# Optimization experiments

Measured on AMD Instinct MI355X. Metric: run time of the kernel, lower is better.

## Reference

```python
import jax, jax.numpy as jnp
import numpy as np

# SemiConv2d with semifield_type='MaxMin':
#   out[n,oc,i,j] = max_{ic,kh,kw} min(x_pad[n,ic,i+kh,j+kw], kernel[oc,ic,kh,kw])
# stride=1, 'same' padding with -inf (identity of max).

def setup_inputs() -> dict:
    key = jax.random.key(0)
    kx, kk = jax.random.split(key)
    x = jax.random.normal(kx, (8, 32, 96, 96), dtype=jnp.float32)
    kernel = jax.random.normal(kk, (32, 32, 3, 3), dtype=jnp.float32)
    return {"x": x, "kernel": kernel}


def reference(x, kernel):
    N, IC, H, W = x.shape
    OC, IC2, KH, KW = kernel.shape
    assert IC == IC2
    # same padding for k=3, stride=1 (left=top=1, right=bottom=1)
    p = KH - 1
    top = left = p // 2
    bot = right = p - top
    xp = jnp.pad(x, ((0, 0), (0, 0), (top, bot), (left, right)),
                 constant_values=-jnp.inf)
    out = None
    # small fixed loop over kernel taps (KH*KW = 9); vectorized over N, OC, IC, H, W
    for kh in range(KH):
        for kw in range(KW):
            win = xp[:, :, kh:kh + H, kw:kw + W]           # [N, IC, H, W]
            k_tap = kernel[:, :, kh, kw]                   # [OC, IC]
            # min over values, max over input channels -> [N, OC, H, W]
            v = jnp.max(jnp.minimum(win[:, None], k_tap[None, :, :, None, None]), axis=2)
            out = v if out is None else jnp.maximum(out, v)
    return out
```

## Files before the change

kernel.cpp:

```cpp
#include <hip/hip_runtime.h>
#include <math.h>
#include <stdint.h>


#define HH 96
#define WW 96
#define CIN 32
#define OCN 32
#define XQ_ROWS 98
#define XQ_W 48
#define XQ_SLICE (XQ_ROWS * XQ_W)
#define XQ_TOTAL (256 * XQ_SLICE)
#define TB_TOTAL (32 * 288)
#define WS_NEED ((size_t)XQ_TOTAL * 8 + (size_t)TB_TOTAL * 16)
#define NEGH2 0xFC00FC00u

typedef _Float16 h2 __attribute__((ext_vector_type(2)));
typedef uint32_t u2a4 __attribute__((ext_vector_type(2), aligned(4)));

__device__ __forceinline__ uint32_t pkmin_vs(uint32_t x, uint32_t k) {
    uint32_t d;
    asm("v_pk_min_f16 %0, %1, %2" : "=v"(d) : "v"(x), "s"(k));
    return d;
}
__device__ __forceinline__ uint32_t pkmin_vv(uint32_t a, uint32_t b) {
    uint32_t d;
    asm("v_pk_min_f16 %0, %1, %2" : "=v"(d) : "v"(a), "v"(b));
    return d;
}
__device__ __forceinline__ uint32_t pkmax(uint32_t a, uint32_t b) {
    uint32_t d;
    asm("v_pk_max_f16 %0, %1, %2" : "=v"(d) : "v"(a), "v"(b));
    return d;
}
__device__ __forceinline__ uint32_t packh2(float lo, float hi) {
    h2 p = {(_Float16)lo, (_Float16)hi};
    return __builtin_bit_cast(uint32_t, p);
}

__global__ __launch_bounds__(256) void setup_xq(const float* __restrict__ x,
                                                uint2* __restrict__ xq) {
    int idx = blockIdx.x * 256 + threadIdx.x;
    int j  = idx % XQ_W;
    int t  = idx / XQ_W;
    int hp = t % XQ_ROWS;
    int s  = t / XQ_ROWS;
    int h  = hp - 1;
    bool hv = (h >= 0) && (h < HH);
    const float* row = x + ((size_t)s * HH + (hv ? h : 0)) * WW;
    float a = (hv && j > 0)        ? row[2 * j - 1] : -INFINITY;
    float b = hv                   ? row[2 * j]     : -INFINITY;
    float c = hv                   ? row[2 * j + 1] : -INFINITY;
    float d = (hv && j < XQ_W - 1) ? row[2 * j + 2] : -INFINITY;
    uint2 v;
    v.x = packh2(a, b);
    v.y = packh2(c, d);
    xq[idx] = v;
}

__global__ void setup_tap(const float* __restrict__ kk, uint4* __restrict__ tbl) {
    __shared__ float ks[288];
    const int oc = blockIdx.x;
    const int t  = threadIdx.x;
    float k = kk[oc * 288 + t];
    ks[t] = k;
    __syncthreads();
    int rank = 0;
    for (int s = 0; s < 288; ++s) {
        float kv = ks[s];
        rank += (kv > k) || (kv == k && s < t);
    }
    const int ic = t / 9, tap = t % 9, dh = tap / 3, dw = tap % 3;
    uint32_t off = (uint32_t)(ic * XQ_ROWS + dh) * (XQ_W * 8) + (dw == 2 ? 4u : 0u);
    uint32_t sh  = (dw == 1) ? 16u : 0u;
    tbl[oc * 288 + rank] = make_uint4(packh2(k, k), off, sh, 0u);
}

__device__ __forceinline__ uint32_t tapval(const char* xb, int vbyte, uint4 e) {
    u2a4 q = *(const u2a4*)(xb + e.y + (uint32_t)vbyte);
    uint32_t v = __builtin_amdgcn_alignbit(q.y, q.x, e.z);
    return pkmin_vs(v, e.x);
}

__global__ __launch_bounds__(192, 8) void semiconv_ee(const char* __restrict__ xqb,
                                                      const uint4* __restrict__ tbl,
                                                      float* __restrict__ out) {
    const int tid = threadIdx.x;
    const int jj = tid % 48;
    const int hr = tid / 48;
    const int b  = blockIdx.x;
    const int hp = b % 24;
    const int t  = b / 24;
    const int oc = t & 31;
    const int n  = t >> 5;
    const int h  = hp * 4 + hr;

    const char* xb = xqb + (size_t)n * CIN * XQ_SLICE * 8;
    const int vbyte = (h * XQ_W + jj) * 8;
    const uint4* tb = tbl + oc * 288;

    uint32_t acc = NEGH2;
    uint4 e0 = tb[0], e1 = tb[1], e2 = tb[2], e3 = tb[3];

    for (int c = 0; c < 72; ++c) {
        uint4 f0, f1, f2, f3;
        if (c < 71) {
            const uint4* nb = tb + 4 * (c + 1);
            f0 = nb[0]; f1 = nb[1]; f2 = nb[2]; f3 = nb[3];
        }
        uint32_t m0 = tapval(xb, vbyte, e0);
        uint32_t m1 = tapval(xb, vbyte, e1);
        uint32_t m2 = tapval(xb, vbyte, e2);
        uint32_t m3 = tapval(xb, vbyte, e3);
        acc = pkmax(acc, pkmax(pkmax(m0, m1), pkmax(m2, m3)));

        if (c < 71) {
            uint32_t sw = __builtin_amdgcn_alignbit(acc, acc, 16);
            uint32_t mn = pkmin_vv(acc, sw);
            h2 a  = __builtin_bit_cast(h2, mn);
            h2 kn = __builtin_bit_cast(h2, f0.x);
            if (__all((float)a.x >= (float)kn.x)) break;
            e0 = f0; e1 = f1; e2 = f2; e3 = f3;
        }
    }

    h2 a = __builtin_bit_cast(h2, acc);
    float2 v = make_float2((float)a.x, (float)a.y);
    *(float2*)(out + (((size_t)(n * OCN + oc)) * HH + h) * WW + 2 * jj) = v;
}

#define NEGINF (-INFINITY)
__global__ __launch_bounds__(192, 8) void semiconv2d_f32(
    const float* __restrict__ x, const float* __restrict__ kk, float* __restrict__ out)
{
    const int tid = threadIdx.x;
    const int w  = tid % WW;
    const int hr = tid / WW;
    const int b   = blockIdx.x;
    const int ocb = b & 7;
    const int hp  = (b >> 3) % 48;
    const int n   = (b >> 3) / 48;
    const int h   = hp * 2 + hr;
    const int oc0 = ocb * 4;
    float a0[4], a1[4], a2[4];
#pragma unroll
    for (int i = 0; i < 4; ++i) { a0[i] = NEGINF; a1[i] = NEGINF; a2[i] = NEGINF; }
    const bool vm = (h > 0), vp = (h < HH - 1);
    const int hm  = vm ? h - 1 : h;
    const int hpl = vp ? h + 1 : h;
    const int cm  = (w > 0) ? -1 : 0;
    const int cp  = (w < WW - 1) ? 1 : 0;
    const float* rm = x + ((size_t)(n * CIN) * HH + hm)  * WW + w;
    const float* r1 = x + ((size_t)(n * CIN) * HH + h)   * WW + w;
    const float* rp = x + ((size_t)(n * CIN) * HH + hpl) * WW + w;
#pragma unroll 2
    for (int ic = 0; ic < CIN; ++ic) {
        float r00 = vm ? rm[cm] : NEGINF, r01 = vm ? rm[0] : NEGINF, r02 = vm ? rm[cp] : NEGINF;
        float r10 = r1[cm], r11 = r1[0], r12 = r1[cp];
        float r20 = vp ? rp[cm] : NEGINF, r21 = vp ? rp[0] : NEGINF, r22 = vp ? rp[cp] : NEGINF;
#pragma unroll
        for (int oc = 0; oc < 4; ++oc) {
            const float* kq = kk + (size_t)(((oc0 + oc) * CIN + ic)) * 9;
            a0[oc] = fmaxf(fmaxf(a0[oc], fminf(r00, kq[0])), fmaxf(fminf(r10, kq[3]), fminf(r20, kq[6])));
            a1[oc] = fmaxf(fmaxf(a1[oc], fminf(r01, kq[1])), fmaxf(fminf(r11, kq[4]), fminf(r21, kq[7])));
            a2[oc] = fmaxf(fmaxf(a2[oc], fminf(r02, kq[2])), fmaxf(fminf(r12, kq[5]), fminf(r22, kq[8])));
        }
        rm += HH * WW; r1 += HH * WW; rp += HH * WW;
    }
#pragma unroll
    for (int oc = 0; oc < 4; ++oc) {
        float v0 = (w > 0)      ? a0[oc] : NEGINF;
        float v2 = (w < WW - 1) ? a2[oc] : NEGINF;
        out[(((size_t)(n * OCN + oc0 + oc)) * HH + h) * WW + w] = fmaxf(fmaxf(v0, a1[oc]), v2);
    }
}

extern "C" void kernel_launch(void* const* d_in, const int* in_sizes, int n_in,
                              void* d_out, int out_size, void* d_ws, size_t ws_size,
                              hipStream_t stream) {
    const float* x  = (const float*)d_in[0];
    const float* kk = (const float*)d_in[1];
    float* out      = (float*)d_out;
    if (ws_size >= WS_NEED) {
        uint2* xq  = (uint2*)d_ws;
        uint4* tbl = (uint4*)((char*)d_ws + (size_t)XQ_TOTAL * 8);
        setup_xq<<<dim3(XQ_TOTAL / 256), dim3(256), 0, stream>>>(x, xq);
        setup_tap<<<dim3(32), dim3(288), 0, stream>>>(kk, tbl);
        semiconv_ee<<<dim3(8 * 32 * 24), dim3(192), 0, stream>>>(
            (const char*)xq, tbl, out);
    } else {
        semiconv2d_f32<<<dim3(8 * 48 * 8), dim3(192), 0, stream>>>(x, kk, out);
    }
}
```

Baseline: 101.6 us.

## Pack tap table to 8 bytes and check early exit every 16 taps

```diff
diff --git a/kernel.cpp b/kernel.cpp
--- a/kernel.cpp
+++ b/kernel.cpp
@@ -12,7 +12,7 @@
 #define XQ_SLICE (XQ_ROWS * XQ_W)
 #define XQ_TOTAL (256 * XQ_SLICE)
 #define TB_TOTAL (32 * 288)
-#define WS_NEED ((size_t)XQ_TOTAL * 8 + (size_t)TB_TOTAL * 16)
+#define WS_NEED ((size_t)XQ_TOTAL * 8 + (size_t)TB_TOTAL * 8)
 #define NEGH2 0xFC00FC00u
 
 typedef _Float16 h2 __attribute__((ext_vector_type(2)));
@@ -58,7 +58,7 @@
     xq[idx] = v;
 }
 
-__global__ void setup_tap(const float* __restrict__ kk, uint4* __restrict__ tbl) {
+__global__ void setup_tap(const float* __restrict__ kk, uint2* __restrict__ tbl) {
     __shared__ float ks[288];
     const int oc = blockIdx.x;
     const int t  = threadIdx.x;
@@ -72,18 +72,12 @@
     }
     const int ic = t / 9, tap = t % 9, dh = tap / 3, dw = tap % 3;
     uint32_t off = (uint32_t)(ic * XQ_ROWS + dh) * (XQ_W * 8) + (dw == 2 ? 4u : 0u);
-    uint32_t sh  = (dw == 1) ? 16u : 0u;
-    tbl[oc * 288 + rank] = make_uint4(packh2(k, k), off, sh, 0u);
-}
-
-__device__ __forceinline__ uint32_t tapval(const char* xb, int vbyte, uint4 e) {
-    u2a4 q = *(const u2a4*)(xb + e.y + (uint32_t)vbyte);
-    uint32_t v = __builtin_amdgcn_alignbit(q.y, q.x, e.z);
-    return pkmin_vs(v, e.x);
+    uint32_t meta = off | (dw == 1 ? 1u : 0u);
+    tbl[oc * 288 + rank] = make_uint2(packh2(k, k), meta);
 }
 
 __global__ __launch_bounds__(192, 8) void semiconv_ee(const char* __restrict__ xqb,
-                                                      const uint4* __restrict__ tbl,
+                                                      const uint2* __restrict__ tbl,
                                                       float* __restrict__ out) {
     const int tid = threadIdx.x;
     const int jj = tid % 48;
@@ -97,30 +91,39 @@
 
     const char* xb = xqb + (size_t)n * CIN * XQ_SLICE * 8;
     const int vbyte = (h * XQ_W + jj) * 8;
-    const uint4* tb = tbl + oc * 288;
+    const uint2* tb = tbl + oc * 288;
 
     uint32_t acc = NEGH2;
-    uint4 e0 = tb[0], e1 = tb[1], e2 = tb[2], e3 = tb[3];
 
-    for (int c = 0; c < 72; ++c) {
-        uint4 f0, f1, f2, f3;
-        if (c < 71) {
-            const uint4* nb = tb + 4 * (c + 1);
-            f0 = nb[0]; f1 = nb[1]; f2 = nb[2]; f3 = nb[3];
+    for (int c = 0; c < 18; ++c) {
+        uint32_t a0 = NEGH2, a1 = NEGH2, a2 = NEGH2, a3 = NEGH2;
+        const uint2* e = tb + c * 16;
+#pragma unroll
+        for (int i = 0; i < 4; ++i) {
+            uint2 e0 = e[4 * i + 0], e1 = e[4 * i + 1];
+            uint2 e2 = e[4 * i + 2], e3 = e[4 * i + 3];
+            uint32_t o0 = e0.y & ~1u, s0 = (e0.y & 1u) << 4;
+            uint32_t o1 = e1.y & ~1u, s1 = (e1.y & 1u) << 4;
+            uint32_t o2 = e2.y & ~1u, s2 = (e2.y & 1u) << 4;
+            uint32_t o3 = e3.y & ~1u, s3 = (e3.y & 1u) << 4;
+            u2a4 q0 = *(const u2a4*)(xb + o0 + (uint32_t)vbyte);
+            u2a4 q1 = *(const u2a4*)(xb + o1 + (uint32_t)vbyte);
+            u2a4 q2 = *(const u2a4*)(xb + o2 + (uint32_t)vbyte);
+            u2a4 q3 = *(const u2a4*)(xb + o3 + (uint32_t)vbyte);
+            a0 = pkmax(a0, pkmin_vs(__builtin_amdgcn_alignbit(q0.y, q0.x, s0), e0.x));
+            a1 = pkmax(a1, pkmin_vs(__builtin_amdgcn_alignbit(q1.y, q1.x, s1), e1.x));
+            a2 = pkmax(a2, pkmin_vs(__builtin_amdgcn_alignbit(q2.y, q2.x, s2), e2.x));
+            a3 = pkmax(a3, pkmin_vs(__builtin_amdgcn_alignbit(q3.y, q3.x, s3), e3.x));
         }
-        uint32_t m0 = tapval(xb, vbyte, e0);
-        uint32_t m1 = tapval(xb, vbyte, e1);
-        uint32_t m2 = tapval(xb, vbyte, e2);
-        uint32_t m3 = tapval(xb, vbyte, e3);
-        acc = pkmax(acc, pkmax(pkmax(m0, m1), pkmax(m2, m3)));
+        acc = pkmax(acc, pkmax(pkmax(a0, a1), pkmax(a2, a3)));
 
-        if (c < 71) {
+        if (c >= 5 && c < 17) {
+            uint32_t kn = tb[16 * (c + 1)].x;
             uint32_t sw = __builtin_amdgcn_alignbit(acc, acc, 16);
             uint32_t mn = pkmin_vv(acc, sw);
-            h2 a  = __builtin_bit_cast(h2, mn);
-            h2 kn = __builtin_bit_cast(h2, f0.x);
-            if (__all((float)a.x >= (float)kn.x)) break;
-            e0 = f0; e1 = f1; e2 = f2; e3 = f3;
+            h2 A  = __builtin_bit_cast(h2, mn);
+            h2 KN = __builtin_bit_cast(h2, kn);
+            if (__all((float)A.x >= (float)KN.x)) break;
         }
     }
 
@@ -183,7 +186,7 @@
     float* out      = (float*)d_out;
     if (ws_size >= WS_NEED) {
         uint2* xq  = (uint2*)d_ws;
-        uint4* tbl = (uint4*)((char*)d_ws + (size_t)XQ_TOTAL * 8);
+        uint2* tbl = (uint2*)((char*)d_ws + (size_t)XQ_TOTAL * 8);
         setup_xq<<<dim3(XQ_TOTAL / 256), dim3(256), 0, stream>>>(x, xq);
         setup_tap<<<dim3(32), dim3(288), 0, stream>>>(kk, tbl);
         semiconv_ee<<<dim3(8 * 32 * 24), dim3(192), 0, stream>>>(
```

Result: slower. 130.2 us (+28.2%).
